# Optimization experiments

Hardware: AMD Instinct MI355X
Metric: run time of the kernel (lower is better)

Reference implementation:

```python
import jax, jax.numpy as jnp
import numpy as np

B, C, H, W = 16, 16, 256, 256
HID, OUT_C, IN_C = 128, 13, 3

_SOBEL_X = np.array([[-1, 0, 1], [-2, 0, 2], [-1, 0, 1]], dtype=np.float32)
_SOBEL_Y = _SOBEL_X.T


def setup_inputs() -> dict:
    key = jax.random.key(0)
    k1, k2, k3, k4 = jax.random.split(key, 4)
    return {
        "input_grid": jax.random.normal(k1, (B, C, H, W), dtype=jnp.float32),
        "w1": jax.random.normal(k2, (HID, 3 * C), dtype=jnp.float32) * 0.0001,
        "b1": jax.random.normal(k3, (HID,), dtype=jnp.float32) * 0.0001,
        "w2": jax.random.normal(k4, (OUT_C, HID), dtype=jnp.float32) * 0.0001,
    }


def _depthwise_sobel(x_padded, filt2d):
    # x_padded: [B, C, H+2, W+2]; depthwise 3x3 valid conv (groups=C)
    c = x_padded.shape[1]
    kern = jnp.broadcast_to(jnp.asarray(filt2d)[None, None], (c, 1, 3, 3))
    return jax.lax.conv_general_dilated(
        x_padded, kern, window_strides=(1, 1), padding="VALID",
        feature_group_count=c,
        dimension_numbers=("NCHW", "OIHW", "NCHW"))


def reference(input_grid, w1, b1, w2):
    # circular pad by 1 on spatial dims
    xp = jnp.pad(input_grid, ((0, 0), (0, 0), (1, 1), (1, 1)), mode="wrap")
    gx = _depthwise_sobel(xp, _SOBEL_X)
    gy = _depthwise_sobel(xp, _SOBEL_Y)
    # perception grid: [B, 3C, H, W]
    perception = jnp.concatenate([input_grid, gx, gy], axis=1)
    # update network: 1x1 conv -> ReLU -> 1x1 conv (dropout = identity in eval)
    h = jax.nn.relu(jnp.einsum("bchw,oc->bohw", perception, w1)
                    + b1[None, :, None, None])
    ds = jnp.einsum("bchw,oc->bohw", h, w2)  # [B, C-IN_C, H, W]
    # residual add to channels 3: of the state
    return input_grid.at[:, IN_C:].add(ds)
```

## Files before the change

### kernel.cpp

```cpp
#include <hip/hip_runtime.h>

#define BB   16
#define CC   16
#define HH   256
#define WW   256
#define HID  128
#define OUTC 13

typedef short short8 __attribute__((ext_vector_type(8)));
typedef float floatx16 __attribute__((ext_vector_type(16)));
typedef float floatx4 __attribute__((ext_vector_type(4)));

__device__ __forceinline__ unsigned short f2bf(float x) {
    unsigned int u = __float_as_uint(x);
    u += 0x7fffu + ((u >> 16) & 1u);
    return (unsigned short)(u >> 16);
}

__device__ __forceinline__ unsigned int cvt_pk_bf16(float lo, float hi) {
    unsigned int d;
    asm("v_cvt_pk_bf16_f32 %0, %1, %2" : "=v"(d) : "v"(lo), "v"(hi));
    return d;
}

#define W1F_BYTES 36864
#define W2F_OFF   36864

__global__ __launch_bounds__(256) void gca_prep(
    const float* __restrict__ w1, const float* __restrict__ w2,
    unsigned char* __restrict__ ws)
{
    const int id = blockIdx.x * 256 + threadIdx.x;
    const float SX[9] = {-1.f, 0.f, 1.f, -2.f, 0.f, 2.f, -1.f, 0.f, 1.f};
    const float SY[9] = {-1.f, -2.f, -1.f, 0.f, 0.f, 0.f, 1.f, 2.f, 1.f};

    if (id < 2304) {
        const int mtG  = id / 576;
        const int rem  = id % 576;
        const int tap  = rem / 64;
        const int lane = rem % 64;
        const int p  = lane & 31, hi = lane >> 5;
        const int hid = 32 * mtG + p;
        const float cen = (tap == 4) ? 1.f : 0.f;
        const float sxv = SX[tap], syv = SY[tap];
        const float* wr = w1 + hid * 48;
        unsigned int o[4];
        for (int k = 0; k < 4; ++k) {
            int c0 = 8 * hi + 2 * k;
            float v0 = wr[c0]     * cen + wr[16 + c0]     * sxv + wr[32 + c0]     * syv;
            float v1 = wr[c0 + 1] * cen + wr[16 + c0 + 1] * sxv + wr[32 + c0 + 1] * syv;
            o[k] = (unsigned int)f2bf(v0) | ((unsigned int)f2bf(v1) << 16);
        }
        *(uint4*)(ws + (size_t)id * 16) = make_uint4(o[0], o[1], o[2], o[3]);
    } else if (id < 2816) {
        const int id2 = id - 2304;
        const int s    = id2 / 64;
        const int lane = id2 % 64;
        const int outc = lane & 31, hi = lane >> 5;
        unsigned int o[4];
        for (int k = 0; k < 4; ++k) {
            int hid0 = 16 * s + 8 * hi + 2 * k;
            float v0 = (outc < OUTC) ? w2[outc * HID + hid0]     : 0.f;
            float v1 = (outc < OUTC) ? w2[outc * HID + hid0 + 1] : 0.f;
            o[k] = (unsigned int)f2bf(v0) | ((unsigned int)f2bf(v1) << 16);
        }
        *(uint4*)(ws + W2F_OFF + (size_t)id2 * 16) = make_uint4(o[0], o[1], o[2], o[3]);
    }
}

#define TILE_DW 6120
#define CB_DW   1024
#define LDS_DW  (TILE_DW + 2 * CB_DW)

__global__ __launch_bounds__(256) void gca_main(
    const float* __restrict__ in,
    const float* __restrict__ b1,
    const unsigned char* __restrict__ ws,
    float* __restrict__ out)
{
    __shared__ unsigned int lds[LDS_DW];

    const int tid  = threadIdx.x;
    const int wid  = tid >> 6;
    const int lane = tid & 63;
    const int hw   = wid & 1;
    const int P    = wid >> 1;
    const int p    = lane & 31;
    const int hi   = lane >> 5;

    const int bI = blockIdx.x >> 7;
    const int rm = blockIdx.x & 127;
    const int y0 = (rm >> 3) << 4;
    const int x0 = (rm & 7)  << 5;

    const float* inb  = in  + ((size_t)bI << 20);
    float*       outb = out + ((size_t)bI << 20);

    {
        int e = tid;
#pragma unroll
        for (int it = 0; it < 2; ++it) {
            if (e < 384) {
                int c = e >> 7, rem = e & 127, rw = rem >> 3, q = rem & 7;
                int idx = (c << 16) + ((y0 + rw) << 8) + x0 + (q << 2);
                *(floatx4*)(outb + idx) = *(const floatx4*)(inb + idx);
            }
            e += 256;
        }
    }

    {
        const int g = tid >> 5, l = tid & 31;
        const float* cp = inb + ((size_t)(2 * g) << 16);
        const int xA = (x0 + l - 1) & 255;
        const int xB = (x0 + l + 31) & 255;
        const int ldsA = l * 10 + g;
        const int ldsB = (l + 32) * 10 + g;
        const bool doB = (l < 2);
        for (int rw = 0; rw < 18; ++rw) {
            const int yo = ((y0 + rw - 1) & 255) << 8;
            float a0 = cp[yo + xA], a1 = cp[yo + xA + 65536];
            lds[rw * 340 + ldsA] = cvt_pk_bf16(a0, a1);
            if (doB) {
                float c0 = cp[yo + xB], c1 = cp[yo + xB + 65536];
                lds[rw * 340 + ldsB] = cvt_pk_bf16(c0, c1);
            }
        }
    }
    __syncthreads();

    const unsigned char* w1f  = ws + ((size_t)(2 * hw) * 9) * 64 * 16;
    const unsigned char* w2fp = ws + W2F_OFF + (size_t)(4 * hw) * 64 * 16;

    short8 a2f[4];
#pragma unroll
    for (int sp = 0; sp < 4; ++sp)
        a2f[sp] = *(const short8*)(w2fp + (size_t)(sp * 64 + lane) * 16);

    int off_[4]; bool val_[4];
#pragma unroll
    for (int j = 0; j < 4; ++j) {
        int r  = 2 * j + hw;
        int oc = (r & 3) + 8 * (r >> 2) + 4 * hi;
        val_[j] = (oc < OUTC);
        off_[j] = (3 + oc) << 16;
    }

    const int mysec = TILE_DW + (P * 2 + hw)       * 256 + 2 * lane;
    const int pasec = TILE_DW + (P * 2 + (1 - hw)) * 256 + 2 * lane;

#pragma unroll 1
    for (int t = 0; t < 8; ++t) {
        const int row   = y0 + 2 * t + P;
        const int ibase = (row << 8) + x0 + p;

        float rs[4];
#pragma unroll
        for (int j = 0; j < 4; ++j)
            rs[j] = val_[j] ? inb[ibase + off_[j]] : 0.f;

        floatx16 acc1[2];
#pragma unroll
        for (int m = 0; m < 2; ++m) {
            const int hb = 64 * hw + 32 * m + 4 * hi;
#pragma unroll
            for (int rr = 0; rr < 4; ++rr) {
                float4 bv = *(const float4*)(b1 + hb + 8 * rr);
                acc1[m][4 * rr + 0] = bv.x;
                acc1[m][4 * rr + 1] = bv.y;
                acc1[m][4 * rr + 2] = bv.z;
                acc1[m][4 * rr + 3] = bv.w;
            }
        }

#pragma unroll
        for (int tap = 0; tap < 9; ++tap) {
            const int tr  = 2 * t + P + tap / 3;
            const int col = p + tap % 3;
            const int dwo = (tr * 34 + col) * 10 + 4 * hi;
            union { unsigned int u[4]; short8 s; } bfr;
            uint2 lo2 = *(const uint2*)&lds[dwo];
            uint2 hi2 = *(const uint2*)&lds[dwo + 2];
            bfr.u[0] = lo2.x; bfr.u[1] = lo2.y; bfr.u[2] = hi2.x; bfr.u[3] = hi2.y;
#pragma unroll
            for (int m = 0; m < 2; ++m) {
                short8 af = *(const short8*)(w1f + (size_t)((m * 9 + tap) * 64 + lane) * 16);
                acc1[m] = __builtin_amdgcn_mfma_f32_32x32x16_bf16(af, bfr.s, acc1[m], 0, 0, 0);
            }
        }

        uint2 hrun[8];
#pragma unroll
        for (int m = 0; m < 2; ++m)
#pragma unroll
            for (int rr = 0; rr < 4; ++rr) {
                float h0 = fmaxf(acc1[m][4 * rr + 0], 0.f);
                float h1 = fmaxf(acc1[m][4 * rr + 1], 0.f);
                float h2 = fmaxf(acc1[m][4 * rr + 2], 0.f);
                float h3 = fmaxf(acc1[m][4 * rr + 3], 0.f);
                hrun[4 * m + rr].x = cvt_pk_bf16(h0, h1);
                hrun[4 * m + rr].y = cvt_pk_bf16(h2, h3);
            }

        floatx16 acc2 = {};
        if (hw == 0) { acc2[0] = rs[0]; acc2[2] = rs[1]; acc2[4] = rs[2]; acc2[6] = rs[3]; }
        else         { acc2[1] = rs[0]; acc2[3] = rs[1]; acc2[5] = rs[2]; acc2[7] = rs[3]; }

#pragma unroll
        for (int sp = 0; sp < 4; ++sp) {
            uint2 r0 = hrun[2 * sp];
            uint2 r1 = hrun[2 * sp + 1];
            uint2 x0s, x1s;
            x0s.x = (unsigned int)__shfl_xor((int)r0.x, 32);
            x0s.y = (unsigned int)__shfl_xor((int)r0.y, 32);
            x1s.x = (unsigned int)__shfl_xor((int)r1.x, 32);
            x1s.y = (unsigned int)__shfl_xor((int)r1.y, 32);
            union { unsigned int u[4]; short8 s; } b2;
            uint2 lo = hi ? x1s : r0;
            uint2 hg = hi ? r1  : x0s;
            b2.u[0] = lo.x; b2.u[1] = lo.y; b2.u[2] = hg.x; b2.u[3] = hg.y;
            acc2 = __builtin_amdgcn_mfma_f32_32x32x16_bf16(a2f[sp], b2.s, acc2, 0, 0, 0);
        }

        const int cb = mysec + (t & 1) * CB_DW;
        uint2 wv0, wv1;
        if (hw == 0) {
            wv0.x = __float_as_uint(acc2[1]); wv0.y = __float_as_uint(acc2[3]);
            wv1.x = __float_as_uint(acc2[5]); wv1.y = __float_as_uint(acc2[7]);
        } else {
            wv0.x = __float_as_uint(acc2[0]); wv0.y = __float_as_uint(acc2[2]);
            wv1.x = __float_as_uint(acc2[4]); wv1.y = __float_as_uint(acc2[6]);
        }
        *(uint2*)&lds[cb]       = wv0;
        *(uint2*)&lds[cb + 128] = wv1;

        __syncthreads();

        const int pb = pasec + (t & 1) * CB_DW;
        uint2 q0 = *(const uint2*)&lds[pb];
        uint2 q1 = *(const uint2*)&lds[pb + 128];

        float s_[4];
        if (hw == 0) {
            s_[0] = acc2[0] + __uint_as_float(q0.x);
            s_[1] = acc2[2] + __uint_as_float(q0.y);
            s_[2] = acc2[4] + __uint_as_float(q1.x);
            s_[3] = acc2[6] + __uint_as_float(q1.y);
        } else {
            s_[0] = acc2[1] + __uint_as_float(q0.x);
            s_[1] = acc2[3] + __uint_as_float(q0.y);
            s_[2] = acc2[5] + __uint_as_float(q1.x);
            s_[3] = acc2[7] + __uint_as_float(q1.y);
        }
#pragma unroll
        for (int j = 0; j < 4; ++j)
            if (val_[j])
                outb[ibase + off_[j]] = s_[j];
    }
}

extern "C" void kernel_launch(void* const* d_in, const int* in_sizes, int n_in,
                              void* d_out, int out_size, void* d_ws, size_t ws_size,
                              hipStream_t stream) {
    const float* x  = (const float*)d_in[0];
    const float* w1 = (const float*)d_in[1];
    const float* b1 = (const float*)d_in[2];
    const float* w2 = (const float*)d_in[3];
    float* out = (float*)d_out;
    unsigned char* ws = (unsigned char*)d_ws;

    hipLaunchKernelGGL(gca_prep, dim3(11), dim3(256), 0, stream, w1, w2, ws);
    hipLaunchKernelGGL(gca_main, dim3(2048), dim3(256), 0, stream, x, b1, ws, out);
}
```

Before: 250.2 us.

## Give each wave a full row's hidden dimension, dropping the cross-wave LDS reduction

Before, two waves split the 128 hidden units of one row and combined their partial second-layer sums through an LDS exchange with a block-wide barrier each iteration. Now each wave computes all 128 hidden units for its own row (4 rows per iteration, 4 iterations) and does the full second matmul itself. This removes the per-iteration __syncthreads, the LDS staging buffers and the redundant partner work. In exchange each wave holds more accumulator registers (four floatx16 for layer 1 plus 16 residual values), and w2 fragments are reloaded from global memory inside the loop, which may reduce occupancy.

```diff
diff --git a/kernel.cpp b/kernel.cpp
--- a/kernel.cpp
+++ b/kernel.cpp
@@ -69,8 +69,6 @@
 }
 
 #define TILE_DW 6120
-#define CB_DW   1024
-#define LDS_DW  (TILE_DW + 2 * CB_DW)
 
 __global__ __launch_bounds__(256) void gca_main(
     const float* __restrict__ in,
@@ -78,13 +76,11 @@
     const unsigned char* __restrict__ ws,
     float* __restrict__ out)
 {
-    __shared__ unsigned int lds[LDS_DW];
+    __shared__ unsigned int lds[TILE_DW];
 
     const int tid  = threadIdx.x;
     const int wid  = tid >> 6;
     const int lane = tid & 63;
-    const int hw   = wid & 1;
-    const int P    = wid >> 1;
     const int p    = lane & 31;
     const int hi   = lane >> 5;
 
@@ -129,40 +125,32 @@
     }
     __syncthreads();
 
-    const unsigned char* w1f  = ws + ((size_t)(2 * hw) * 9) * 64 * 16;
-    const unsigned char* w2fp = ws + W2F_OFF + (size_t)(4 * hw) * 64 * 16;
-
-    short8 a2f[4];
-#pragma unroll
-    for (int sp = 0; sp < 4; ++sp)
-        a2f[sp] = *(const short8*)(w2fp + (size_t)(sp * 64 + lane) * 16);
-
-    int off_[4]; bool val_[4];
-#pragma unroll
-    for (int j = 0; j < 4; ++j) {
-        int r  = 2 * j + hw;
+    const unsigned char* w1f = ws;
+    const unsigned char* w2f = ws + W2F_OFF;
+
+    int off16[16]; bool val16[16];
+#pragma unroll
+    for (int r = 0; r < 16; ++r) {
         int oc = (r & 3) + 8 * (r >> 2) + 4 * hi;
-        val_[j] = (oc < OUTC);
-        off_[j] = (3 + oc) << 16;
-    }
-
-    const int mysec = TILE_DW + (P * 2 + hw)       * 256 + 2 * lane;
-    const int pasec = TILE_DW + (P * 2 + (1 - hw)) * 256 + 2 * lane;
+        val16[r] = (oc < OUTC);
+        off16[r] = (3 + oc) << 16;
+    }
 
 #pragma unroll 1
-    for (int t = 0; t < 8; ++t) {
-        const int row   = y0 + 2 * t + P;
+    for (int t = 0; t < 4; ++t) {
+        const int rr4   = 4 * t + wid;
+        const int row   = y0 + rr4;
         const int ibase = (row << 8) + x0 + p;
 
-        float rs[4];
-#pragma unroll
-        for (int j = 0; j < 4; ++j)
-            rs[j] = val_[j] ? inb[ibase + off_[j]] : 0.f;
-
-        floatx16 acc1[2];
-#pragma unroll
-        for (int m = 0; m < 2; ++m) {
-            const int hb = 64 * hw + 32 * m + 4 * hi;
+        float rs[16];
+#pragma unroll
+        for (int r = 0; r < 16; ++r)
+            rs[r] = val16[r] ? inb[ibase + off16[r]] : 0.f;
+
+        floatx16 acc1[4];
+#pragma unroll
+        for (int m = 0; m < 4; ++m) {
+            const int hb = 32 * m + 4 * hi;
 #pragma unroll
             for (int rr = 0; rr < 4; ++rr) {
                 float4 bv = *(const float4*)(b1 + hb + 8 * rr);
@@ -175,7 +163,7 @@
 
 #pragma unroll
         for (int tap = 0; tap < 9; ++tap) {
-            const int tr  = 2 * t + P + tap / 3;
+            const int tr  = rr4 + tap / 3;
             const int col = p + tap % 3;
             const int dwo = (tr * 34 + col) * 10 + 4 * hi;
             union { unsigned int u[4]; short8 s; } bfr;
@@ -183,15 +171,15 @@
             uint2 hi2 = *(const uint2*)&lds[dwo + 2];
             bfr.u[0] = lo2.x; bfr.u[1] = lo2.y; bfr.u[2] = hi2.x; bfr.u[3] = hi2.y;
 #pragma unroll
-            for (int m = 0; m < 2; ++m) {
+            for (int m = 0; m < 4; ++m) {
                 short8 af = *(const short8*)(w1f + (size_t)((m * 9 + tap) * 64 + lane) * 16);
                 acc1[m] = __builtin_amdgcn_mfma_f32_32x32x16_bf16(af, bfr.s, acc1[m], 0, 0, 0);
             }
         }
 
-        uint2 hrun[8];
-#pragma unroll
-        for (int m = 0; m < 2; ++m)
+        uint2 hrun[16];
+#pragma unroll
+        for (int m = 0; m < 4; ++m)
 #pragma unroll
             for (int rr = 0; rr < 4; ++rr) {
                 float h0 = fmaxf(acc1[m][4 * rr + 0], 0.f);
@@ -202,12 +190,12 @@
                 hrun[4 * m + rr].y = cvt_pk_bf16(h2, h3);
             }
 
-        floatx16 acc2 = {};
-        if (hw == 0) { acc2[0] = rs[0]; acc2[2] = rs[1]; acc2[4] = rs[2]; acc2[6] = rs[3]; }
-        else         { acc2[1] = rs[0]; acc2[3] = rs[1]; acc2[5] = rs[2]; acc2[7] = rs[3]; }
-
-#pragma unroll
-        for (int sp = 0; sp < 4; ++sp) {
+        floatx16 acc2;
+#pragma unroll
+        for (int r = 0; r < 16; ++r) acc2[r] = rs[r];
+
+#pragma unroll
+        for (int sp = 0; sp < 8; ++sp) {
             uint2 r0 = hrun[2 * sp];
             uint2 r1 = hrun[2 * sp + 1];
             uint2 x0s, x1s;
@@ -219,43 +207,14 @@
             uint2 lo = hi ? x1s : r0;
             uint2 hg = hi ? r1  : x0s;
             b2.u[0] = lo.x; b2.u[1] = lo.y; b2.u[2] = hg.x; b2.u[3] = hg.y;
-            acc2 = __builtin_amdgcn_mfma_f32_32x32x16_bf16(a2f[sp], b2.s, acc2, 0, 0, 0);
-        }
-
-        const int cb = mysec + (t & 1) * CB_DW;
-        uint2 wv0, wv1;
-        if (hw == 0) {
-            wv0.x = __float_as_uint(acc2[1]); wv0.y = __float_as_uint(acc2[3]);
-            wv1.x = __float_as_uint(acc2[5]); wv1.y = __float_as_uint(acc2[7]);
-        } else {
-            wv0.x = __float_as_uint(acc2[0]); wv0.y = __float_as_uint(acc2[2]);
-            wv1.x = __float_as_uint(acc2[4]); wv1.y = __float_as_uint(acc2[6]);
-        }
-        *(uint2*)&lds[cb]       = wv0;
-        *(uint2*)&lds[cb + 128] = wv1;
-
-        __syncthreads();
-
-        const int pb = pasec + (t & 1) * CB_DW;
-        uint2 q0 = *(const uint2*)&lds[pb];
-        uint2 q1 = *(const uint2*)&lds[pb + 128];
-
-        float s_[4];
-        if (hw == 0) {
-            s_[0] = acc2[0] + __uint_as_float(q0.x);
-            s_[1] = acc2[2] + __uint_as_float(q0.y);
-            s_[2] = acc2[4] + __uint_as_float(q1.x);
-            s_[3] = acc2[6] + __uint_as_float(q1.y);
-        } else {
-            s_[0] = acc2[1] + __uint_as_float(q0.x);
-            s_[1] = acc2[3] + __uint_as_float(q0.y);
-            s_[2] = acc2[5] + __uint_as_float(q1.x);
-            s_[3] = acc2[7] + __uint_as_float(q1.y);
-        }
-#pragma unroll
-        for (int j = 0; j < 4; ++j)
-            if (val_[j])
-                outb[ibase + off_[j]] = s_[j];
+            short8 a2 = *(const short8*)(w2f + (size_t)(sp * 64 + lane) * 16);
+            acc2 = __builtin_amdgcn_mfma_f32_32x32x16_bf16(a2, b2.s, acc2, 0, 0, 0);
+        }
+
+#pragma unroll
+        for (int r = 0; r < 16; ++r)
+            if (val16[r])
+                outb[ibase + off16[r]] = acc2[r];
     }
 }
 
```

After: 291.3 us. +16.4%, slower.
